# Kernel optimization log

Measured on AMD Instinct MI355X. Metric: run time of the kernel, lower is better.

## Reference

```python
import jax, jax.numpy as jnp
import numpy as np

B, N, H = 512, 100, 768
I = 2 * H  # intermediate_dim default = hidden_dim * 2
NUM_ANS = 16
MAX_ANS = 15
LN_EPS = 1e-5


def setup_inputs() -> dict:
    key = jax.random.key(0)
    ks = jax.random.split(key, 7)
    s = 0.02
    return {
        "v_emb": jax.random.normal(ks[0], (B, N, H), dtype=jnp.float32),
        "W1": jax.random.normal(ks[1], (H, I), dtype=jnp.float32) * s,
        "b1": jax.random.normal(ks[2], (I,), dtype=jnp.float32) * s,
        "gamma": jnp.ones((I,), dtype=jnp.float32),
        "beta": jnp.zeros((I,), dtype=jnp.float32),
        "W2": jax.random.normal(ks[3], (I, 1), dtype=jnp.float32) * s,
        "b2": jax.random.normal(ks[4], (1,), dtype=jnp.float32) * s,
    }


def reference(v_emb, W1, b1, gamma, beta, W2, b2):
    # Linear -> GELU (exact/erf, torch nn.GELU default) -> LayerNorm -> Linear
    h = jnp.einsum("bnh,hi->bni", v_emb, W1) + b1            # [B,N,I]
    h = jax.nn.gelu(h, approximate=False)
    mu = jnp.mean(h, axis=-1, keepdims=True)
    var = jnp.mean(jnp.square(h - mu), axis=-1, keepdims=True)
    h = (h - mu) * jax.lax.rsqrt(var + LN_EPS) * gamma + beta
    scores = jnp.einsum("bni,io->bno", h, W2) + b2           # [B,N,1]
    scores = jax.nn.sigmoid(scores)                           # sigmoid=True branch
    pred = jnp.sum(scores, axis=1)                            # [B,1]
    # pred_to_logits: vectorized round + clamp + one-hot scatter
    # str(int(round(p))) in {'0'..'15'} -> that id; negative -> 0; overflow -> max_ans
    aid = jnp.clip(jnp.round(pred[:, 0]).astype(jnp.int32), 0, MAX_ANS)
    logits = jax.nn.one_hot(aid, NUM_ANS, dtype=scores.dtype)  # [B,16]
    # original returns dict: scores, final_attention_map (==scores), pred, logits
    return scores, pred, logits
```

## Files before the change

kernel.cpp:

```cpp
#include <hip/hip_runtime.h>
#include <hip/hip_bf16.h>
#include <cstdint>
#include <cstddef>

#define BB   512
#define NN   100
#define HH   768
#define II   1536
#define MM   (BB*NN)

typedef __bf16 bf16;
typedef __bf16 bf16x4 __attribute__((ext_vector_type(4)));
typedef __bf16 bf16x8 __attribute__((ext_vector_type(8)));
typedef float  f32x4  __attribute__((ext_vector_type(4)));

__device__ __forceinline__ void gld_lds16(const void* g, void* l) {
    __builtin_amdgcn_global_load_lds(
        (const __attribute__((address_space(1))) void*)g,
        (__attribute__((address_space(3))) void*)l, 16, 0, 0);
}

template <int PAT>
__device__ __forceinline__ float swz_add(float x) {
    return x + __int_as_float(
        __builtin_amdgcn_ds_swizzle(__float_as_int(x), PAT));
}
__device__ __forceinline__ float red16(float x) {
    x = swz_add<0x041F>(x);
    x = swz_add<0x081F>(x);
    x = swz_add<0x101F>(x);
    x = swz_add<0x201F>(x);
    return x;
}

__device__ __forceinline__ float fast_gelu(float x) {
    const float ax = fabsf(x) * 0.70710678118654752f;
    const float t  = __builtin_amdgcn_rcpf(fmaf(0.3275911f, ax, 1.0f));
    float p = fmaf(1.061405429f, t, -1.453152027f);
    p = fmaf(p, t, 1.421413741f);
    p = fmaf(p, t, -0.284496736f);
    p = fmaf(p, t, 0.254829592f);
    p = p * t;
    const float e    = __expf(-ax * ax);
    const float erfa = fmaf(-p, e, 1.0f);
    const float erfx = copysignf(erfa, x);
    return 0.5f * x * (1.0f + erfx);
}

__global__ __launch_bounds__(256) void prep_kernel(
    const float* __restrict__ W1, const float* __restrict__ gamma,
    const float* __restrict__ beta, const float* __restrict__ W2,
    const float* __restrict__ b2,
    bf16* __restrict__ Wp, float* __restrict__ gw, float* __restrict__ scal)
{
    const int bid = blockIdx.x, tid = threadIdx.x;
    if (bid < 288) {
        __shared__ bf16 Ts[64 * 72];
        const int kt = bid % 12, nt = bid / 12;
        const int k0 = kt * 64, n0 = nt * 64;
        #pragma unroll
        for (int it = 0; it < 4; ++it) {
            const int idx = it * 256 + tid;
            const int r   = idx >> 4;
            const int c4  = idx & 15;
            float4 v = *(const float4*)&W1[(size_t)(k0 + r) * II + n0 + c4*4];
            Ts[(c4*4 + 0) * 72 + r] = (bf16)v.x;
            Ts[(c4*4 + 1) * 72 + r] = (bf16)v.y;
            Ts[(c4*4 + 2) * 72 + r] = (bf16)v.z;
            Ts[(c4*4 + 3) * 72 + r] = (bf16)v.w;
        }
        __syncthreads();
        #pragma unroll
        for (int it = 0; it < 2; ++it) {
            const int idx = it * 256 + tid;
            const int nr  = idx >> 3;
            const int kc  = idx & 7;
            *(bf16x8*)&Wp[(size_t)(n0 + nr) * HH + k0 + kc*8]
                = *(const bf16x8*)&Ts[nr * 72 + kc*8];
        }
    } else if (bid == 288) {
        for (int j = tid; j < II; j += 256)
            gw[j] = gamma[j] * W2[j];
    } else {
        float s1 = 0.f, s2 = 0.f;
        for (int j = tid; j < II; j += 256) {
            float w2 = W2[j];
            s1 += gamma[j] * w2;
            s2 += beta[j]  * w2;
        }
        #pragma unroll
        for (int off = 32; off; off >>= 1) {
            s1 += __shfl_down(s1, off, 64);
            s2 += __shfl_down(s2, off, 64);
        }
        __shared__ float a1[4], a2[4];
        int lane = tid & 63, w = tid >> 6;
        if (lane == 0) { a1[w] = s1; a2[w] = s2; }
        __syncthreads();
        if (tid == 0) {
            scal[0] = a1[0] + a1[1] + a1[2] + a1[3];
            scal[1] = a2[0] + a2[1] + a2[2] + a2[3] + b2[0];
        }
    }
}

__global__ __launch_bounds__(256) void gemm_part(
    const float* __restrict__ Af, const bf16* __restrict__ Wp,
    const float* __restrict__ b1, const float* __restrict__ gw,
    float* __restrict__ part)
{
    __shared__ float AsF[128 * 64];
    __shared__ bf16  Bs[128 * 64];

    const int tid  = threadIdx.x;
    const int lin  = (blockIdx.x % 8) * 600 + blockIdx.x / 8;
    const int mb   = lin / 12;
    const int nb   = lin % 12;
    const int lane = tid & 63;
    const int w    = tid >> 6;
    const int wm   = w >> 1;
    const int wn   = w & 1;
    const int m15  = lane & 15;
    const int q    = lane >> 4;
    const int row0 = mb * 128;

    const int ar = tid >> 4;
    const int h  = tid & 15;
    const int ap = h >> 1;
    const int asl = ap ^ (ar & 7);
    const float* aP = Af + (size_t)(row0 + ar) * HH + asl * 8 + (h & 1) * 4;

    const int br = tid >> 3;
    const int bsl = (tid & 7) ^ (br & 7);
    const bf16* bP = Wp + (size_t)(nb*128 + br) * HH + bsl * 8;

    f32x4 acc[4][4] = {};

    for (int kt = 0; kt < 12; ++kt) {
        #pragma unroll
        for (int it = 0; it < 4; ++it)
            gld_lds16(bP + (size_t)it * 32 * HH, &Bs[tid*8 + it*2048]);
        #pragma unroll
        for (int it = 0; it < 8; ++it)
            gld_lds16(aP + (size_t)it * 16 * HH, &AsF[tid*4 + it*1024]);
        asm volatile("s_waitcnt vmcnt(0)" ::: "memory");
        __syncthreads();

        #pragma unroll
        for (int kb = 0; kb < 2; ++kb) {
            const int pk_ = kb * 4 + q;
            bf16x8 af[4], bfr[4];
            #pragma unroll
            for (int mt = 0; mt < 4; ++mt) {
                const int rr = wm*64 + mt*16 + m15;
                const int fb = rr * 64 + (pk_ ^ (rr & 7)) * 8;
                f32x4 lo = *(const f32x4*)&AsF[fb];
                f32x4 hi = *(const f32x4*)&AsF[fb + 4];
                af[mt] = bf16x8{ (bf16)lo[0], (bf16)lo[1], (bf16)lo[2],
                                 (bf16)lo[3], (bf16)hi[0], (bf16)hi[1],
                                 (bf16)hi[2], (bf16)hi[3] };
            }
            const int swz = (pk_ ^ (m15 & 7)) * 8;
            #pragma unroll
            for (int nt = 0; nt < 4; ++nt)
                bfr[nt] = *(const bf16x8*)&Bs[(wn*64 + nt*16 + m15) * 64 + swz];
            #pragma unroll
            for (int mt = 0; mt < 4; ++mt)
                #pragma unroll
                for (int nt = 0; nt < 4; ++nt)
                    acc[mt][nt] = __builtin_amdgcn_mfma_f32_16x16x32_bf16(
                        af[mt], bfr[nt], acc[mt][nt], 0, 0, 0);
        }
        __syncthreads();
        aP += 64; bP += 64;
    }

    float* sred = (float*)Bs;

    float bv[4], gv[4];
    #pragma unroll
    for (int nt = 0; nt < 4; ++nt) {
        const int col = nb*128 + wn*64 + nt*16 + m15;
        bv[nt] = b1[col];
        gv[nt] = gw[col];
    }

    #pragma unroll
    for (int mt = 0; mt < 4; ++mt) {
        #pragma unroll
        for (int r = 0; r < 4; ++r) {
            float x0 = 0.f, x1 = 0.f, x2 = 0.f;
            #pragma unroll
            for (int nt = 0; nt < 4; ++nt) {
                float g = fast_gelu(acc[mt][nt][r] + bv[nt]);
                x0 += g; x1 += g * g; x2 += g * gv[nt];
            }
            x0 = red16(x0); x1 = red16(x1); x2 = red16(x2);
            if (m15 == 0) {
                const int rl = wm*64 + mt*16 + q*4 + r;
                sred[wn*384 + rl*3 + 0] = x0;
                sred[wn*384 + rl*3 + 1] = x1;
                sred[wn*384 + rl*3 + 2] = x2;
            }
        }
    }
    __syncthreads();

    if (tid < 128) {
        const size_t rg = (size_t)row0 + tid;
        #pragma unroll
        for (int s = 0; s < 3; ++s)
            part[(size_t)s * 12 * MM + (size_t)nb * MM + rg]
                = sred[0*384 + tid*3 + s] + sred[1*384 + tid*3 + s];
    }
}

__global__ __launch_bounds__(128) void score_pred(
    const float* __restrict__ part, const float* __restrict__ scal,
    float* __restrict__ o_scores, float* __restrict__ o_pred,
    float* __restrict__ o_logits)
{
    const int b = blockIdx.x, t = threadIdx.x;
    float s = 0.f;
    if (t < NN) {
        const size_t row = (size_t)b * NN + t;
        float Sh = 0.f, Shh = 0.f, Shg = 0.f;
        #pragma unroll
        for (int j = 0; j < 12; ++j) {
            Sh  += part[(size_t)0*12*MM + (size_t)j*MM + row];
            Shh += part[(size_t)1*12*MM + (size_t)j*MM + row];
            Shg += part[(size_t)2*12*MM + (size_t)j*MM + row];
        }
        const float mu   = Sh * (1.0f / II);
        const float var  = Shh * (1.0f / II) - mu * mu;
        const float rstd = rsqrtf(var + 1e-5f);
        const float z    = rstd * (Shg - mu * scal[0]) + scal[1];
        s = 1.0f / (1.0f + __expf(-z));
        o_scores[row] = s;
    }
    float v = s;
    #pragma unroll
    for (int off = 32; off; off >>= 1) v += __shfl_down(v, off, 64);
    __shared__ float ssum[2];
    const int lane = t & 63, w = t >> 6;
    if (lane == 0) ssum[w] = v;
    __syncthreads();
    const float p = ssum[0] + ssum[1];
    if (t == 0) o_pred[b] = p;
    if (t < 16) {
        int aid = (int)rintf(p);
        aid = aid < 0 ? 0 : (aid > 15 ? 15 : aid);
        o_logits[b * 16 + t] = (t == aid) ? 1.0f : 0.0f;
    }
}

extern "C" void kernel_launch(void* const* d_in, const int* in_sizes, int n_in,
                              void* d_out, int out_size, void* d_ws, size_t ws_size,
                              hipStream_t stream)
{
    const float* v_emb = (const float*)d_in[0];
    const float* W1    = (const float*)d_in[1];
    const float* b1    = (const float*)d_in[2];
    const float* gamma = (const float*)d_in[3];
    const float* beta  = (const float*)d_in[4];
    const float* W2    = (const float*)d_in[5];
    const float* b2    = (const float*)d_in[6];

    char* ws = (char*)d_ws;
    size_t off = 0;
    bf16*  Wp   = (bf16*)(ws + off);  off += (size_t)II * HH * 2;
    float* gw   = (float*)(ws + off); off += (size_t)II * 4;
    float* scal = (float*)(ws + off); off += 256;
    float* part = (float*)(ws + off); off += (size_t)MM * 36 * 4;

    float* out       = (float*)d_out;
    float* o_scores  = out;
    float* o_pred    = out + MM;
    float* o_logits  = out + MM + BB;

    hipLaunchKernelGGL(prep_kernel, dim3(290), dim3(256), 0, stream,
                       W1, gamma, beta, W2, b2, Wp, gw, scal);
    hipLaunchKernelGGL(gemm_part, dim3((MM / 128) * 12), dim3(256),
                       0, stream, v_emb, Wp, b1, gw, part);
    hipLaunchKernelGGL(score_pred, dim3(BB), dim3(128), 0, stream,
                       part, scal, o_scores, o_pred, o_logits);
}
```

Baseline: 459.5 us.

## Pre-convert activations to bf16 in prep kernel before the GEMM

Adds 9600 blocks to the prep kernel that convert v_emb from fp32 to bf16 into a workspace buffer. The GEMM then loads A as bf16 through the same swizzled LDS path as B, which halves A's LDS footprint and drops the per-iteration fp32-to-bf16 conversion inside the inner loop. The trade is an extra pass over the 157MB input: a full fp32 read plus a 78MB bf16 write. Each of the 12 column-tile blocks that re-read A now reads half the bytes.

```diff
diff --git a/kernel.cpp b/kernel.cpp
--- a/kernel.cpp
+++ b/kernel.cpp
@@ -50,11 +50,21 @@
 __global__ __launch_bounds__(256) void prep_kernel(
     const float* __restrict__ W1, const float* __restrict__ gamma,
     const float* __restrict__ beta, const float* __restrict__ W2,
-    const float* __restrict__ b2,
-    bf16* __restrict__ Wp, float* __restrict__ gw, float* __restrict__ scal)
+    const float* __restrict__ b2, const float* __restrict__ A,
+    bf16* __restrict__ Wp, float* __restrict__ gw, float* __restrict__ scal,
+    bf16* __restrict__ Apk)
 {
     const int bid = blockIdx.x, tid = threadIdx.x;
-    if (bid < 288) {
+    if (bid >= 290) {
+        const size_t base = (size_t)(bid - 290) * 4096 + tid * 4;
+        #pragma unroll
+        for (int it = 0; it < 4; ++it) {
+            const size_t i = base + it * 1024;
+            float4 v = *(const float4*)&A[i];
+            bf16x4 o = { (bf16)v.x, (bf16)v.y, (bf16)v.z, (bf16)v.w };
+            *(bf16x4*)&Apk[i] = o;
+        }
+    } else if (bid < 288) {
         __shared__ bf16 Ts[64 * 72];
         const int kt = bid % 12, nt = bid / 12;
         const int k0 = kt * 64, n0 = nt * 64;
@@ -105,12 +115,12 @@
 }
 
 __global__ __launch_bounds__(256) void gemm_part(
-    const float* __restrict__ Af, const bf16* __restrict__ Wp,
+    const bf16* __restrict__ Apk, const bf16* __restrict__ Wp,
     const float* __restrict__ b1, const float* __restrict__ gw,
     float* __restrict__ part)
 {
-    __shared__ float AsF[128 * 64];
-    __shared__ bf16  Bs[128 * 64];
+    __shared__ bf16 As[128 * 64];
+    __shared__ bf16 Bs[128 * 64];
 
     const int tid  = threadIdx.x;
     const int lin  = (blockIdx.x % 8) * 600 + blockIdx.x / 8;
@@ -124,43 +134,31 @@
     const int q    = lane >> 4;
     const int row0 = mb * 128;
 
-    const int ar = tid >> 4;
-    const int h  = tid & 15;
-    const int ap = h >> 1;
-    const int asl = ap ^ (ar & 7);
-    const float* aP = Af + (size_t)(row0 + ar) * HH + asl * 8 + (h & 1) * 4;
-
-    const int br = tid >> 3;
-    const int bsl = (tid & 7) ^ (br & 7);
-    const bf16* bP = Wp + (size_t)(nb*128 + br) * HH + bsl * 8;
+    const int rsub  = tid >> 3;
+    const int kg    = (tid & 7) ^ (rsub & 7);
+    const int lbase = tid * 8;
+
+    const bf16* aP = Apk + (size_t)(row0    + rsub) * HH + kg * 8;
+    const bf16* bP = Wp  + (size_t)(nb*128 + rsub) * HH + kg * 8;
 
     f32x4 acc[4][4] = {};
 
     for (int kt = 0; kt < 12; ++kt) {
         #pragma unroll
-        for (int it = 0; it < 4; ++it)
-            gld_lds16(bP + (size_t)it * 32 * HH, &Bs[tid*8 + it*2048]);
-        #pragma unroll
-        for (int it = 0; it < 8; ++it)
-            gld_lds16(aP + (size_t)it * 16 * HH, &AsF[tid*4 + it*1024]);
+        for (int it = 0; it < 4; ++it) {
+            gld_lds16(aP + (size_t)it * 32 * HH, &As[lbase + it * 2048]);
+            gld_lds16(bP + (size_t)it * 32 * HH, &Bs[lbase + it * 2048]);
+        }
         asm volatile("s_waitcnt vmcnt(0)" ::: "memory");
         __syncthreads();
 
         #pragma unroll
         for (int kb = 0; kb < 2; ++kb) {
-            const int pk_ = kb * 4 + q;
+            const int swz = (((kb * 4 + q) ^ (m15 & 7)) * 8);
             bf16x8 af[4], bfr[4];
             #pragma unroll
-            for (int mt = 0; mt < 4; ++mt) {
-                const int rr = wm*64 + mt*16 + m15;
-                const int fb = rr * 64 + (pk_ ^ (rr & 7)) * 8;
-                f32x4 lo = *(const f32x4*)&AsF[fb];
-                f32x4 hi = *(const f32x4*)&AsF[fb + 4];
-                af[mt] = bf16x8{ (bf16)lo[0], (bf16)lo[1], (bf16)lo[2],
-                                 (bf16)lo[3], (bf16)hi[0], (bf16)hi[1],
-                                 (bf16)hi[2], (bf16)hi[3] };
-            }
-            const int swz = (pk_ ^ (m15 & 7)) * 8;
+            for (int mt = 0; mt < 4; ++mt)
+                af[mt] = *(const bf16x8*)&As[(wm*64 + mt*16 + m15) * 64 + swz];
             #pragma unroll
             for (int nt = 0; nt < 4; ++nt)
                 bfr[nt] = *(const bf16x8*)&Bs[(wn*64 + nt*16 + m15) * 64 + swz];
@@ -175,7 +173,7 @@
         aP += 64; bP += 64;
     }
 
-    float* sred = (float*)Bs;
+    float* sred = (float*)As;
 
     float bv[4], gv[4];
     #pragma unroll
@@ -272,16 +270,17 @@
     float* gw   = (float*)(ws + off); off += (size_t)II * 4;
     float* scal = (float*)(ws + off); off += 256;
     float* part = (float*)(ws + off); off += (size_t)MM * 36 * 4;
+    bf16*  Apk  = (bf16*)(ws + off);  off += (size_t)MM * HH * 2;
 
     float* out       = (float*)d_out;
     float* o_scores  = out;
     float* o_pred    = out + MM;
     float* o_logits  = out + MM + BB;
 
-    hipLaunchKernelGGL(prep_kernel, dim3(290), dim3(256), 0, stream,
-                       W1, gamma, beta, W2, b2, Wp, gw, scal);
+    hipLaunchKernelGGL(prep_kernel, dim3(290 + 9600), dim3(256), 0, stream,
+                       W1, gamma, beta, W2, b2, v_emb, Wp, gw, scal, Apk);
     hipLaunchKernelGGL(gemm_part, dim3((MM / 128) * 12), dim3(256),
-                       0, stream, v_emb, Wp, b1, gw, part);
+                       0, stream, Apk, Wp, b1, gw, part);
     hipLaunchKernelGGL(score_pred, dim3(BB), dim3(128), 0, stream,
                        part, scal, o_scores, o_pred, o_logits);
 }
```

New measurement: 428.1 us. 1.07x faster.
